# Performance work log

Hardware: AMD Instinct MI355X
Metric: run time of the kernel (lower is better)

The kernel has to match this reference:

```python
import jax, jax.numpy as jnp
import numpy as np

MASK_VALUE = 0.0  # default `mask=0` scalar in the original forward


def setup_inputs() -> dict:
    key = jax.random.key(0)
    kq, kk, kv = jax.random.split(key, 3)
    b, n, d_k, d_v = 8, 2048, 64, 64
    q = jax.random.normal(kq, (b, n, d_k), dtype=jnp.float32)
    k = jax.random.normal(kk, (b, n, d_k), dtype=jnp.float32)
    v = jax.random.normal(kv, (b, n, d_v), dtype=jnp.float32)
    return {"q": q, "k": k, "v": v}


def reference(q, k, v):
    d_k = q.shape[-1]
    temper = jnp.asarray(d_k, q.dtype) ** 0.5
    # scores: (b, n, n)
    attn = jnp.einsum('bqd,bkd->bqk', q, k) / temper
    # equality-based masking: positions whose score exactly equals the
    # scalar `mask` (default 0) are set to -inf before softmax.
    attn = jnp.where(attn == MASK_VALUE, -jnp.inf, attn)
    # NOTE: the original code calls `attn.masked_fill(look_ahead_mask==0, -inf)`
    # WITHOUT assignment, so the look-ahead mask is a no-op; we omit it faithfully.
    attn = jax.nn.softmax(attn, axis=-1)
    out = jnp.einsum('bqk,bkd->bqd', attn, v)  # (b, n, d_v)
    return out
```

## Files before the change

### kernel.cpp

```cpp
#include <hip/hip_runtime.h>
#include <hip/hip_bf16.h>

typedef __bf16 bf16_t;
typedef bf16_t bf16x2 __attribute__((ext_vector_type(2)));
typedef bf16_t bf16x8 __attribute__((ext_vector_type(8)));
typedef float  floatx4  __attribute__((ext_vector_type(4)));
typedef float  floatx16 __attribute__((ext_vector_type(16)));

constexpr int B = 8, N = 2048, D = 64;

__global__ __launch_bounds__(256)
void prepass_kernel(const float* __restrict__ k, const float* __restrict__ v,
                    bf16_t* __restrict__ kf, bf16_t* __restrict__ vf) {
    __shared__ float t[32 * 65];
    const int tid = threadIdx.x;
    const int b   = blockIdx.x & 7;
    const int kvb = blockIdx.x >> 3;
    const size_t inoff  = ((size_t)b * N + kvb * 32) * D;
    const size_t outoff = (size_t)(b * 64 + kvb) * 2048;

    {
        const float* src = k + inoff;
        floatx4 f0 = *(const floatx4*)(src + tid * 8);
        floatx4 f1 = *(const floatx4*)(src + tid * 8 + 4);
        bf16x8 o;
        #pragma unroll
        for (int j = 0; j < 4; ++j) { o[j] = (bf16_t)f0[j]; o[j + 4] = (bf16_t)f1[j]; }
        const int rr = tid >> 3, kd = (tid >> 1) & 3, hh = tid & 1;
        *(bf16x8*)(kf + outoff + (size_t)kd * 512 + (hh * 32 + rr) * 8) = o;
    }
    {
        const float* src = v + inoff;
        floatx4 f0 = *(const floatx4*)(src + tid * 8);
        floatx4 f1 = *(const floatx4*)(src + tid * 8 + 4);
        const int rr = tid >> 3, cc = (tid & 7) * 8;
        #pragma unroll
        for (int j = 0; j < 4; ++j) { t[rr * 65 + cc + j] = f0[j]; t[rr * 65 + cc + 4 + j] = f1[j]; }
        __syncthreads();
        const int s2 = tid >> 7, dblk = (tid >> 6) & 1, lane = tid & 63;
        const int hh = lane >> 5, l31 = lane & 31;
        bf16x8 o;
        #pragma unroll
        for (int j = 0; j < 8; ++j)
            o[j] = (bf16_t)t[(s2 * 16 + hh * 8 + j) * 65 + dblk * 32 + l31];
        *(bf16x8*)(vf + outoff + (size_t)(s2 * 2 + dblk) * 512 + lane * 8) = o;
    }
}

__global__ __launch_bounds__(512, 4)
void attn_kernel(const float* __restrict__ q, const bf16_t* __restrict__ kf,
                 const bf16_t* __restrict__ vf, float* __restrict__ out) {
    __shared__ char smem[58240];
    float* o_buf = (float*)smem;
    float* l_buf = (float*)(smem + 57344);

    const int tid  = threadIdx.x;
    const int lane = tid & 63;
    const int cg   = tid >> 6;
    const int h    = lane >> 5;
    const int l31  = lane & 31;

    const int b  = blockIdx.x & 7;
    const int q0 = (blockIdx.x >> 3) * 32;

    const bf16_t* kfb = kf + (size_t)b * 131072;
    const bf16_t* vfb = vf + (size_t)b * 131072;

    bf16x8 qf[4];
    {
        const float* qp = q + ((size_t)b * N + q0 + l31) * D + h * 8;
        #pragma unroll
        for (int kd = 0; kd < 4; ++kd) {
            floatx4 f0 = *(const floatx4*)(qp + kd * 16);
            floatx4 f1 = *(const floatx4*)(qp + kd * 16 + 4);
            bf16x8 t;
            #pragma unroll
            for (int j = 0; j < 4; ++j) {
                t[j]     = (bf16_t)(f0[j] * 0.125f);
                t[j + 4] = (bf16_t)(f1[j] * 0.125f);
            }
            qf[kd] = t;
        }
    }

    floatx16 o_acc[2];
    #pragma unroll
    for (int d = 0; d < 2; ++d)
        #pragma unroll
        for (int i = 0; i < 16; ++i) o_acc[d][i] = 0.f;
    float l_run = 0.f;

    bf16x8 kreg[4];
    #pragma unroll
    for (int kd = 0; kd < 4; ++kd)
        kreg[kd] = *(const bf16x8*)(kfb + (size_t)cg * 2048 + kd * 512 + lane * 8);

    #pragma unroll 2
    for (int it = 0; it < 8; ++it) {
        const size_t base = (size_t)(it * 8 + cg) * 2048;

        bf16x8 vreg[4];
        #pragma unroll
        for (int u = 0; u < 4; ++u)
            vreg[u] = *(const bf16x8*)(vfb + base + (size_t)u * 512 + lane * 8);

        floatx16 s;
        #pragma unroll
        for (int i = 0; i < 16; ++i) s[i] = 0.f;
        #pragma unroll
        for (int kd = 0; kd < 4; ++kd)
            s = __builtin_amdgcn_mfma_f32_32x32x16_bf16(kreg[kd], qf[kd], s, 0, 0, 0);

        if (it + 1 < 8) {
            const size_t nbase = (size_t)((it + 1) * 8 + cg) * 2048;
            #pragma unroll
            for (int kd = 0; kd < 4; ++kd)
                kreg[kd] = *(const bf16x8*)(kfb + nbase + (size_t)kd * 512 + lane * 8);
        }

        int q8[8];
        #pragma unroll
        for (int g = 0; g < 8; ++g) {
            union { int i; bf16x2 h2; } u;
            #pragma unroll
            for (int j = 0; j < 2; ++j) {
                float x = s[2 * g + j];
                float p = (x == 0.0f) ? 0.0f : __expf(x);
                l_run += p;
                u.h2[j] = (bf16_t)p;
            }
            q8[g] = u.i;
        }

        #pragma unroll
        for (int s2 = 0; s2 < 2; ++s2) {
            int r0 = __shfl_xor(q8[4 * s2 + 0], 32);
            int r1 = __shfl_xor(q8[4 * s2 + 1], 32);
            int r2 = __shfl_xor(q8[4 * s2 + 2], 32);
            int r3 = __shfl_xor(q8[4 * s2 + 3], 32);
            union { int i4[4]; bf16x8 v; } bf;
            bf.i4[0] = h ? r2 : q8[4 * s2 + 0];
            bf.i4[1] = h ? r3 : q8[4 * s2 + 1];
            bf.i4[2] = h ? q8[4 * s2 + 2] : r0;
            bf.i4[3] = h ? q8[4 * s2 + 3] : r1;
            #pragma unroll
            for (int dblk = 0; dblk < 2; ++dblk)
                o_acc[dblk] = __builtin_amdgcn_mfma_f32_32x32x16_bf16(vreg[s2 * 2 + dblk], bf.v,
                                                                      o_acc[dblk], 0, 0, 0);
        }
    }

    l_run += __shfl_xor(l_run, 32);

    if (cg > 0) {
        float* ob = o_buf + (size_t)(cg - 1) * 2048;
        #pragma unroll
        for (int dblk = 0; dblk < 2; ++dblk)
            #pragma unroll
            for (int i = 0; i < 16; ++i) {
                const int d = (i & 3) + 8 * (i >> 2) + 4 * h + dblk * 32;
                ob[d * 32 + l31] = o_acc[dblk][i];
            }
        if (h == 0) l_buf[(cg - 1) * 32 + l31] = l_run;
    }
    __syncthreads();
    if (cg == 0) {
        float lsum = l_run;
        #pragma unroll
        for (int gg = 0; gg < 7; ++gg) lsum += l_buf[gg * 32 + l31];
        const float inv_l = 1.0f / lsum;
        float* op = out + ((size_t)b * N + q0 + l31) * D;
        #pragma unroll
        for (int dblk = 0; dblk < 2; ++dblk)
            #pragma unroll
            for (int g = 0; g < 4; ++g) {
                const int d0 = 8 * g + 4 * h + dblk * 32;
                floatx4 o4;
                #pragma unroll
                for (int j = 0; j < 4; ++j) {
                    float sum = o_acc[dblk][4 * g + j];
                    #pragma unroll
                    for (int gg = 0; gg < 7; ++gg)
                        sum += o_buf[(size_t)gg * 2048 + (d0 + j) * 32 + l31];
                    o4[j] = sum * inv_l;
                }
                *(floatx4*)(op + d0) = o4;
            }
    }
}

extern "C" void kernel_launch(void* const* d_in, const int* in_sizes, int n_in,
                              void* d_out, int out_size, void* d_ws, size_t ws_size,
                              hipStream_t stream) {
    const float* q = (const float*)d_in[0];
    const float* k = (const float*)d_in[1];
    const float* v = (const float*)d_in[2];
    float* out = (float*)d_out;
    bf16_t* kfrag = (bf16_t*)d_ws;
    bf16_t* vfrag = (bf16_t*)((char*)d_ws + (size_t)B * N * D * 2);

    hipLaunchKernelGGL(prepass_kernel, dim3(512), dim3(256), 0, stream, k, v, kfrag, vfrag);
    hipLaunchKernelGGL(attn_kernel, dim3(512), dim3(512), 0, stream, q, kfrag, vfrag, out);
}
```

Before: 81.87 us.

## Use exp2 with folded log2e, permlane32 swap, setprio, and parallel final reduction

Folds log2(e) into the Q scale so the softmax can use the hardware exp2 directly, and splits the row-sum accumulator into two chains. Replaces the four cross-half shuffles and selects with two permlane32_swap ops, and raises wave priority around the MFMA blocks. The final cross-wave reduction now has every wave store its partials to LDS so that all 8 waves each reduce and write one slice of the output, instead of wave 0 doing all of it. This costs more LDS (the extra buffer for wave 0), and folding the scale before rounding Q to bf16 slightly changes which scores land exactly on zero.

```diff
diff --git a/kernel.cpp b/kernel.cpp
--- a/kernel.cpp
+++ b/kernel.cpp
@@ -6,6 +6,7 @@
 typedef bf16_t bf16x8 __attribute__((ext_vector_type(8)));
 typedef float  floatx4  __attribute__((ext_vector_type(4)));
 typedef float  floatx16 __attribute__((ext_vector_type(16)));
+typedef int    intx2    __attribute__((ext_vector_type(2)));
 
 constexpr int B = 8, N = 2048, D = 64;
 
@@ -50,9 +51,8 @@
 __global__ __launch_bounds__(512, 4)
 void attn_kernel(const float* __restrict__ q, const bf16_t* __restrict__ kf,
                  const bf16_t* __restrict__ vf, float* __restrict__ out) {
-    __shared__ char smem[58240];
-    float* o_buf = (float*)smem;
-    float* l_buf = (float*)(smem + 57344);
+    __shared__ float o_buf[8 * 2048];
+    __shared__ float l_buf[8 * 32];
 
     const int tid  = threadIdx.x;
     const int lane = tid & 63;
@@ -66,6 +66,7 @@
     const bf16_t* kfb = kf + (size_t)b * 131072;
     const bf16_t* vfb = vf + (size_t)b * 131072;
 
+    constexpr float QSCALE = 0.125f * 1.4426950408889634f;
     bf16x8 qf[4];
     {
         const float* qp = q + ((size_t)b * N + q0 + l31) * D + h * 8;
@@ -76,8 +77,8 @@
             bf16x8 t;
             #pragma unroll
             for (int j = 0; j < 4; ++j) {
-                t[j]     = (bf16_t)(f0[j] * 0.125f);
-                t[j + 4] = (bf16_t)(f1[j] * 0.125f);
+                t[j]     = (bf16_t)(f0[j] * QSCALE);
+                t[j + 4] = (bf16_t)(f1[j] * QSCALE);
             }
             qf[kd] = t;
         }
@@ -88,7 +89,7 @@
     for (int d = 0; d < 2; ++d)
         #pragma unroll
         for (int i = 0; i < 16; ++i) o_acc[d][i] = 0.f;
-    float l_run = 0.f;
+    float l_run0 = 0.f, l_run1 = 0.f;
 
     bf16x8 kreg[4];
     #pragma unroll
@@ -107,9 +108,11 @@
         floatx16 s;
         #pragma unroll
         for (int i = 0; i < 16; ++i) s[i] = 0.f;
+        __builtin_amdgcn_s_setprio(1);
         #pragma unroll
         for (int kd = 0; kd < 4; ++kd)
             s = __builtin_amdgcn_mfma_f32_32x32x16_bf16(kreg[kd], qf[kd], s, 0, 0, 0);
+        __builtin_amdgcn_s_setprio(0);
 
         if (it + 1 < 8) {
             const size_t nbase = (size_t)((it + 1) * 8 + cg) * 2048;
@@ -122,38 +125,44 @@
         #pragma unroll
         for (int g = 0; g < 8; ++g) {
             union { int i; bf16x2 h2; } u;
-            #pragma unroll
-            for (int j = 0; j < 2; ++j) {
-                float x = s[2 * g + j];
-                float p = (x == 0.0f) ? 0.0f : __expf(x);
-                l_run += p;
-                u.h2[j] = (bf16_t)p;
+            {
+                float x = s[2 * g + 0];
+                float p = (x == 0.0f) ? 0.0f : __builtin_amdgcn_exp2f(x);
+                l_run0 += p;
+                u.h2[0] = (bf16_t)p;
+            }
+            {
+                float x = s[2 * g + 1];
+                float p = (x == 0.0f) ? 0.0f : __builtin_amdgcn_exp2f(x);
+                l_run1 += p;
+                u.h2[1] = (bf16_t)p;
             }
             q8[g] = u.i;
         }
 
         #pragma unroll
         for (int s2 = 0; s2 < 2; ++s2) {
-            int r0 = __shfl_xor(q8[4 * s2 + 0], 32);
-            int r1 = __shfl_xor(q8[4 * s2 + 1], 32);
-            int r2 = __shfl_xor(q8[4 * s2 + 2], 32);
-            int r3 = __shfl_xor(q8[4 * s2 + 3], 32);
+            intx2 p02 = __builtin_amdgcn_permlane32_swap(q8[4 * s2 + 0], q8[4 * s2 + 2], false, false);
+            intx2 p13 = __builtin_amdgcn_permlane32_swap(q8[4 * s2 + 1], q8[4 * s2 + 3], false, false);
             union { int i4[4]; bf16x8 v; } bf;
-            bf.i4[0] = h ? r2 : q8[4 * s2 + 0];
-            bf.i4[1] = h ? r3 : q8[4 * s2 + 1];
-            bf.i4[2] = h ? q8[4 * s2 + 2] : r0;
-            bf.i4[3] = h ? q8[4 * s2 + 3] : r1;
+            bf.i4[0] = p02[0];
+            bf.i4[1] = p13[0];
+            bf.i4[2] = p02[1];
+            bf.i4[3] = p13[1];
+            __builtin_amdgcn_s_setprio(1);
             #pragma unroll
             for (int dblk = 0; dblk < 2; ++dblk)
                 o_acc[dblk] = __builtin_amdgcn_mfma_f32_32x32x16_bf16(vreg[s2 * 2 + dblk], bf.v,
                                                                       o_acc[dblk], 0, 0, 0);
-        }
-    }
-
+            __builtin_amdgcn_s_setprio(0);
+        }
+    }
+
+    float l_run = l_run0 + l_run1;
     l_run += __shfl_xor(l_run, 32);
 
-    if (cg > 0) {
-        float* ob = o_buf + (size_t)(cg - 1) * 2048;
+    {
+        float* ob = o_buf + cg * 2048;
         #pragma unroll
         for (int dblk = 0; dblk < 2; ++dblk)
             #pragma unroll
@@ -161,31 +170,25 @@
                 const int d = (i & 3) + 8 * (i >> 2) + 4 * h + dblk * 32;
                 ob[d * 32 + l31] = o_acc[dblk][i];
             }
-        if (h == 0) l_buf[(cg - 1) * 32 + l31] = l_run;
+        if (h == 0) l_buf[cg * 32 + l31] = l_run;
     }
     __syncthreads();
-    if (cg == 0) {
-        float lsum = l_run;
-        #pragma unroll
-        for (int gg = 0; gg < 7; ++gg) lsum += l_buf[gg * 32 + l31];
+    {
+        const int dblk = cg >> 2, g = cg & 3;
+        const int d0 = 8 * g + 4 * h + dblk * 32;
+        float lsum = 0.f;
+        #pragma unroll
+        for (int w = 0; w < 8; ++w) lsum += l_buf[w * 32 + l31];
         const float inv_l = 1.0f / lsum;
-        float* op = out + ((size_t)b * N + q0 + l31) * D;
-        #pragma unroll
-        for (int dblk = 0; dblk < 2; ++dblk)
-            #pragma unroll
-            for (int g = 0; g < 4; ++g) {
-                const int d0 = 8 * g + 4 * h + dblk * 32;
-                floatx4 o4;
-                #pragma unroll
-                for (int j = 0; j < 4; ++j) {
-                    float sum = o_acc[dblk][4 * g + j];
-                    #pragma unroll
-                    for (int gg = 0; gg < 7; ++gg)
-                        sum += o_buf[(size_t)gg * 2048 + (d0 + j) * 32 + l31];
-                    o4[j] = sum * inv_l;
-                }
-                *(floatx4*)(op + d0) = o4;
-            }
+        floatx4 o4;
+        #pragma unroll
+        for (int j = 0; j < 4; ++j) {
+            float sum = 0.f;
+            #pragma unroll
+            for (int w = 0; w < 8; ++w) sum += o_buf[w * 2048 + (d0 + j) * 32 + l31];
+            o4[j] = sum * inv_l;
+        }
+        *(floatx4*)(out + ((size_t)b * N + q0 + l31) * D + d0) = o4;
     }
 }
 
```

New measurement: 80.68 us, median of 2. No clear change (-1.5%).
